# Optimization experiments

Measured on AMD Instinct MI355X. Metric: run time of the kernel, lower is better.

Reference implementation:

```python
import jax, jax.numpy as jnp
import numpy as np

E = 1_000_000
C = 32
OUT = 64


def setup_inputs() -> dict:
    key = jax.random.key(0)
    k_x, k_nb, k_w, k_b = jax.random.split(key, 4)
    x = jax.random.normal(k_x, (E, C), dtype=jnp.float32)
    neighbors = jax.random.randint(k_nb, (E, 4), 0, E, dtype=jnp.int64)
    # Linear(5*C, OUT): weight [OUT, 5C], bias [OUT] (torch layout)
    bound = 1.0 / np.sqrt(5 * C)
    W = jax.random.uniform(k_w, (OUT, 5 * C), minval=-bound, maxval=bound, dtype=jnp.float32)
    b = jax.random.uniform(k_b, (OUT,), minval=-bound, maxval=bound, dtype=jnp.float32)
    return {"x": x, "neighbors": neighbors, "W": W, "b": b}


def reference(x, neighbors, W, b):
    # pad with a zero row so index -1 (clamped to 0 then masked) yields zeros
    padded = jnp.concatenate([x, jnp.zeros((1, x.shape[1]), dtype=x.dtype)], axis=0)
    safe = jnp.clip(neighbors, 0, None)
    nb = padded[safe]                                  # [E, 4, C]
    nb = jnp.where((neighbors < 0)[..., None], 0.0, nb)
    a0, a1, b0, b1 = nb[:, 0], nb[:, 1], nb[:, 2], nb[:, 3]
    desc_a = jnp.concatenate([a0 + a1, jnp.abs(a0 - a1)], axis=1)   # [E, 2C]
    desc_b = jnp.concatenate([b0 + b1, jnp.abs(b0 - b1)], axis=1)   # [E, 2C]
    combined = jnp.concatenate([x, desc_a + desc_b, jnp.abs(desc_a - desc_b)], axis=1)  # [E, 5C]
    return combined @ W.T + b
```

## Files before the change

### kernel.cpp

```cpp
#include <hip/hip_runtime.h>


typedef __bf16 bf16_t;
typedef __bf16 bf16x8 __attribute__((ext_vector_type(8)));
typedef float  f32x4  __attribute__((ext_vector_type(4)));

#define EC      1000000
#define CCH     32
#define OUTD    64
#define KD      160
#define MT      64
#define NTILES  (EC / MT)
#define NFRAG   1280
#define TSTR    68
#define GRID    1024

__global__ __launch_bounds__(256)
void meshconv_kernel(const float* __restrict__ x,
                     const int*   __restrict__ nbr,
                     const float* __restrict__ W,
                     const float* __restrict__ bias,
                     float*       __restrict__ out)
{
    __shared__ bf16_t w_lds[NFRAG * 8];
    __shared__ __attribute__((aligned(16))) float t_lds[4 * 16 * TSTR];

    const int tid  = threadIdx.x;
    const int wave = tid >> 6;
    const int lane = tid & 63;
    const int col  = lane & 15;
    const int quad = lane >> 4;

    for (int i = tid; i < NFRAG; i += 256) {
        const int fc  = i & 15;
        const int fq  = (i >> 4) & 3;
        const int ftn = (i >> 6) & 3;
        const int fks = i >> 8;
        const float* src = W + (ftn * 16 + fc) * KD + fks * 32 + fq * 8;
        f32x4 w0 = *(const f32x4*)src;
        f32x4 w1 = *(const f32x4*)(src + 4);
        bf16x8 wf;
        wf[0]=(bf16_t)w0[0]; wf[1]=(bf16_t)w0[1]; wf[2]=(bf16_t)w0[2]; wf[3]=(bf16_t)w0[3];
        wf[4]=(bf16_t)w1[0]; wf[5]=(bf16_t)w1[1]; wf[6]=(bf16_t)w1[2]; wf[7]=(bf16_t)w1[3];
        *(bf16x8*)&w_lds[i * 8] = wf;
    }

    float bv[4];
#pragma unroll
    for (int tn = 0; tn < 4; ++tn) bv[tn] = bias[tn * 16 + col];

    float* tw = &t_lds[wave * 16 * TSTR];

    __syncthreads();

    auto load_tile = [&](int t, int4& nb, f32x4* buf) {
        const int e = t * MT + wave * 16 + col;
        nb = ((const int4*)nbr)[e];
        const int i0 = nb.x < 0 ? 0 : nb.x;
        const int i1 = nb.y < 0 ? 0 : nb.y;
        const int i2 = nb.z < 0 ? 0 : nb.z;
        const int i3 = nb.w < 0 ? 0 : nb.w;
        const int co = quad * 8;
        const f32x4* p;
        p = (const f32x4*)(x + (size_t)e  * CCH + co); buf[0] = p[0]; buf[1] = p[1];
        p = (const f32x4*)(x + (size_t)i0 * CCH + co); buf[2] = p[0]; buf[3] = p[1];
        p = (const f32x4*)(x + (size_t)i1 * CCH + co); buf[4] = p[0]; buf[5] = p[1];
        p = (const f32x4*)(x + (size_t)i2 * CCH + co); buf[6] = p[0]; buf[7] = p[1];
        p = (const f32x4*)(x + (size_t)i3 * CCH + co); buf[8] = p[0]; buf[9] = p[1];
    };

    int tile = blockIdx.x;
    int4  nbc;
    f32x4 cb[10];
    if (tile < NTILES) load_tile(tile, nbc, cb);

    for (; tile < NTILES; tile += GRID) {
        const int nxt = tile + GRID;
        int4  nbn;
        f32x4 pb[10];
        if (nxt < NTILES) load_tile(nxt, nbn, pb);

        const float m0 = nbc.x < 0 ? 0.f : 1.f;
        const float m1 = nbc.y < 0 ? 0.f : 1.f;
        const float m2 = nbc.z < 0 ? 0.f : 1.f;
        const float m3 = nbc.w < 0 ? 0.f : 1.f;

        bf16x8 af[5];
#pragma unroll
        for (int h = 0; h < 2; ++h) {
#pragma unroll
            for (int j = 0; j < 4; ++j) {
                const int jj = h * 4 + j;
                const float va0 = cb[2 + h][j] * m0;
                const float va1 = cb[4 + h][j] * m1;
                const float vb0 = cb[6 + h][j] * m2;
                const float vb1 = cb[8 + h][j] * m3;
                const float sa = va0 + va1;
                const float da = fabsf(va0 - va1);
                const float sb = vb0 + vb1;
                const float db = fabsf(vb0 - vb1);
                af[0][jj] = (bf16_t)cb[h][j];
                af[1][jj] = (bf16_t)(sa + sb);
                af[2][jj] = (bf16_t)(da + db);
                af[3][jj] = (bf16_t)fabsf(sa - sb);
                af[4][jj] = (bf16_t)fabsf(da - db);
            }
        }

        f32x4 acc[4] = {{0.f,0.f,0.f,0.f},{0.f,0.f,0.f,0.f},
                        {0.f,0.f,0.f,0.f},{0.f,0.f,0.f,0.f}};
#pragma unroll
        for (int ks = 0; ks < 5; ++ks) {
#pragma unroll
            for (int tn = 0; tn < 4; ++tn) {
                const bf16x8 bfr = *(const bf16x8*)&w_lds[(((ks*4+tn)*4+quad)*16 + col) * 8];
                acc[tn] = __builtin_amdgcn_mfma_f32_16x16x32_bf16(af[ks], bfr, acc[tn], 0, 0, 0);
            }
        }

#pragma unroll
        for (int tn = 0; tn < 4; ++tn)
#pragma unroll
            for (int r = 0; r < 4; ++r)
                tw[(quad * 4 + r) * TSTR + tn * 16 + col] = acc[tn][r] + bv[tn];

#pragma unroll
        for (int r = 0; r < 4; ++r) {
            const f32x4 v = *(const f32x4*)&tw[(quad * 4 + r) * TSTR + col * 4];
            float* op = out + (size_t)(tile * MT + wave * 16 + quad * 4 + r) * OUTD + col * 4;
            __builtin_nontemporal_store(v, (f32x4*)op);
        }

        nbc = nbn;
#pragma unroll
        for (int k = 0; k < 10; ++k) cb[k] = pb[k];
    }
}

extern "C" void kernel_launch(void* const* d_in, const int* in_sizes, int n_in,
                              void* d_out, int out_size, void* d_ws, size_t ws_size,
                              hipStream_t stream) {
    const float* x    = (const float*)d_in[0];
    const int*   nbr  = (const int*)d_in[1];
    const float* W    = (const float*)d_in[2];
    const float* bias = (const float*)d_in[3];
    float* out = (float*)d_out;
    meshconv_kernel<<<dim3(GRID), dim3(256), 0, stream>>>(x, nbr, W, bias, out);
}
```

Measured before the change: 410.9 us.

## Pre-convert x to fp16 in workspace and gather half-width rows

Adds a pre-pass kernel that converts x to fp16 in the workspace. The main kernel then gathers 64-byte rows instead of 128-byte rows, which halves the bytes moved by the random neighbor gathers. The MFMA operands are swapped so each lane holds output rows directly, removing the LDS transpose before the stores, and bias is preloaded into the accumulators. In exchange it adds a full extra read/write pass over x and a second launch, and it loses precision from storing x in fp16. The old fp32 kernel is kept as a fallback when the workspace is too small.

Result: slower. 667.7 us (+62.5%).

```diff
diff --git a/kernel.cpp b/kernel.cpp
--- a/kernel.cpp
+++ b/kernel.cpp
@@ -1,19 +1,160 @@
 #include <hip/hip_runtime.h>
 
 
-typedef __bf16 bf16_t;
-typedef __bf16 bf16x8 __attribute__((ext_vector_type(8)));
-typedef float  f32x4  __attribute__((ext_vector_type(4)));
-
-#define EC      1000000
-#define CCH     32
-#define OUTD    64
-#define KD      160
-#define MT      64
-#define NTILES  (EC / MT)
-#define NFRAG   1280
-#define TSTR    68
-#define GRID    1024
+typedef __bf16    bf16_t;
+typedef __bf16    bf16x8 __attribute__((ext_vector_type(8)));
+typedef _Float16  f16_t;
+typedef _Float16  f16x8  __attribute__((ext_vector_type(8)));
+typedef float     f32x4  __attribute__((ext_vector_type(4)));
+
+#define EC        1000000
+#define CCH       32
+#define OUTD      64
+#define KD        160
+#define MT        64
+#define NTILES    (EC / MT)
+#define NFRAG     1280
+#define GRID_F16  1536
+#define CVT_GRID  2048
+#define TSTR      68
+#define GRID_F32  1024
+
+__global__ __launch_bounds__(256)
+void cvt_x_f16(const float* __restrict__ x, f16_t* __restrict__ xh)
+{
+    const size_t n8     = (size_t)EC * CCH / 8;
+    const size_t stride = (size_t)CVT_GRID * 256;
+    size_t i = (size_t)blockIdx.x * 256 + threadIdx.x;
+    for (; i < n8; i += stride) {
+        const f32x4* p = (const f32x4*)x + 2 * i;
+        f32x4 a = __builtin_nontemporal_load(p);
+        f32x4 b = __builtin_nontemporal_load(p + 1);
+        f16x8 h;
+        h[0]=(f16_t)a[0]; h[1]=(f16_t)a[1]; h[2]=(f16_t)a[2]; h[3]=(f16_t)a[3];
+        h[4]=(f16_t)b[0]; h[5]=(f16_t)b[1]; h[6]=(f16_t)b[2]; h[7]=(f16_t)b[3];
+        *((f16x8*)xh + i) = h;
+    }
+}
+
+__global__ __launch_bounds__(256, 6)
+void meshconv_f16(const f16_t* __restrict__ xh,
+                  const int*   __restrict__ nbr,
+                  const float* __restrict__ W,
+                  const float* __restrict__ bias,
+                  float*       __restrict__ out)
+{
+    __shared__ bf16_t w_lds[NFRAG * 8];
+    __shared__ __attribute__((aligned(16))) float b_lds[OUTD];
+
+    const int tid  = threadIdx.x;
+    const int wave = tid >> 6;
+    const int lane = tid & 63;
+    const int col  = lane & 15;
+    const int quad = lane >> 4;
+
+    for (int i = tid; i < NFRAG; i += 256) {
+        const int fc  = i & 15;
+        const int fq  = (i >> 4) & 3;
+        const int ftn = (i >> 6) & 3;
+        const int fks = i >> 8;
+        const float* src = W + (ftn * 16 + fc) * KD + fks * 32 + fq * 8;
+        f32x4 w0 = *(const f32x4*)src;
+        f32x4 w1 = *(const f32x4*)(src + 4);
+        bf16x8 wf;
+        wf[0]=(bf16_t)w0[0]; wf[1]=(bf16_t)w0[1]; wf[2]=(bf16_t)w0[2]; wf[3]=(bf16_t)w0[3];
+        wf[4]=(bf16_t)w1[0]; wf[5]=(bf16_t)w1[1]; wf[6]=(bf16_t)w1[2]; wf[7]=(bf16_t)w1[3];
+        *(bf16x8*)&w_lds[i * 8] = wf;
+    }
+    if (tid < 16) *(f32x4*)&b_lds[tid * 4] = ((const f32x4*)bias)[tid];
+
+    __syncthreads();
+
+    auto ld_nbr = [&](int t) -> int4 {
+        return ((const int4*)nbr)[t * MT + wave * 16 + col];
+    };
+    auto gather = [&](int t, const int4& nb, f16x8* buf) {
+        const int e  = t * MT + wave * 16 + col;
+        const int i0 = nb.x < 0 ? 0 : nb.x;
+        const int i1 = nb.y < 0 ? 0 : nb.y;
+        const int i2 = nb.z < 0 ? 0 : nb.z;
+        const int i3 = nb.w < 0 ? 0 : nb.w;
+        const int co = quad * 8;
+        buf[0] = *(const f16x8*)(xh + (size_t)e  * CCH + co);
+        buf[1] = *(const f16x8*)(xh + (size_t)i0 * CCH + co);
+        buf[2] = *(const f16x8*)(xh + (size_t)i1 * CCH + co);
+        buf[3] = *(const f16x8*)(xh + (size_t)i2 * CCH + co);
+        buf[4] = *(const f16x8*)(xh + (size_t)i3 * CCH + co);
+    };
+
+    int tile = blockIdx.x;
+    int4  nb_cur, nb_nxt;
+    f16x8 cb[5];
+    if (tile < NTILES) {
+        nb_cur = ld_nbr(tile);
+        gather(tile, nb_cur, cb);
+        const int t1 = (tile + GRID_F16 < NTILES) ? tile + GRID_F16 : tile;
+        nb_nxt = ld_nbr(t1);
+    }
+
+    for (; tile < NTILES; tile += GRID_F16) {
+        const int nxt = tile + GRID_F16;
+        f16x8 pb[5];
+        int4  nb2 = nb_nxt;
+        if (nxt < NTILES) {
+            gather(nxt, nb_nxt, pb);
+            const int t2 = (nxt + GRID_F16 < NTILES) ? nxt + GRID_F16 : nxt;
+            nb2 = ld_nbr(t2);
+        }
+
+        const float m0 = nb_cur.x < 0 ? 0.f : 1.f;
+        const float m1 = nb_cur.y < 0 ? 0.f : 1.f;
+        const float m2 = nb_cur.z < 0 ? 0.f : 1.f;
+        const float m3 = nb_cur.w < 0 ? 0.f : 1.f;
+
+        bf16x8 af[5];
+#pragma unroll
+        for (int jj = 0; jj < 8; ++jj) {
+            const float va0 = (float)cb[1][jj] * m0;
+            const float va1 = (float)cb[2][jj] * m1;
+            const float vb0 = (float)cb[3][jj] * m2;
+            const float vb1 = (float)cb[4][jj] * m3;
+            const float sa = va0 + va1;
+            const float da = fabsf(va0 - va1);
+            const float sb = vb0 + vb1;
+            const float db = fabsf(vb0 - vb1);
+            af[0][jj] = (bf16_t)(float)cb[0][jj];
+            af[1][jj] = (bf16_t)(sa + sb);
+            af[2][jj] = (bf16_t)(da + db);
+            af[3][jj] = (bf16_t)fabsf(sa - sb);
+            af[4][jj] = (bf16_t)fabsf(da - db);
+        }
+
+        f32x4 acc[4];
+#pragma unroll
+        for (int tn = 0; tn < 4; ++tn)
+            acc[tn] = *(const f32x4*)&b_lds[tn * 16 + quad * 4];
+#pragma unroll
+        for (int ks = 0; ks < 5; ++ks) {
+#pragma unroll
+            for (int tn = 0; tn < 4; ++tn) {
+                const bf16x8 wfr = *(const bf16x8*)&w_lds[(((ks*4+tn)*4+quad)*16 + col) * 8];
+                acc[tn] = __builtin_amdgcn_mfma_f32_16x16x32_bf16(wfr, af[ks], acc[tn], 0, 0, 0);
+            }
+        }
+
+        {
+            float* ob = out + (size_t)(tile * MT + wave * 16 + col) * OUTD + quad * 4;
+#pragma unroll
+            for (int tn = 0; tn < 4; ++tn)
+                __builtin_nontemporal_store(acc[tn], (f32x4*)(ob + tn * 16));
+        }
+
+        nb_cur = nb_nxt;
+        nb_nxt = nb2;
+#pragma unroll
+        for (int k = 0; k < 5; ++k) cb[k] = pb[k];
+    }
+}
 
 __global__ __launch_bounds__(256)
 void meshconv_kernel(const float* __restrict__ x,
@@ -74,11 +215,11 @@
     f32x4 cb[10];
     if (tile < NTILES) load_tile(tile, nbc, cb);
 
-    for (; tile < NTILES; tile += GRID) {
-        const int nxt = tile + GRID;
+    for (; tile < NTILES; tile += GRID_F32) {
+        const int nxt = tile + GRID_F32;
         int4  nbn;
-        f32x4 pb[10];
-        if (nxt < NTILES) load_tile(nxt, nbn, pb);
+        f32x4 pbuf[10];
+        if (nxt < NTILES) load_tile(nxt, nbn, pbuf);
 
         const float m0 = nbc.x < 0 ? 0.f : 1.f;
         const float m1 = nbc.y < 0 ? 0.f : 1.f;
@@ -133,7 +274,7 @@
 
         nbc = nbn;
 #pragma unroll
-        for (int k = 0; k < 10; ++k) cb[k] = pb[k];
+        for (int k = 0; k < 10; ++k) cb[k] = pbuf[k];
     }
 }
 
@@ -145,5 +286,13 @@
     const float* W    = (const float*)d_in[2];
     const float* bias = (const float*)d_in[3];
     float* out = (float*)d_out;
-    meshconv_kernel<<<dim3(GRID), dim3(256), 0, stream>>>(x, nbr, W, bias, out);
-}
+
+    const size_t need = (size_t)EC * CCH * sizeof(f16_t);
+    if (d_ws != nullptr && ws_size >= need) {
+        f16_t* xh = (f16_t*)d_ws;
+        cvt_x_f16<<<dim3(CVT_GRID), dim3(256), 0, stream>>>(x, xh);
+        meshconv_f16<<<dim3(GRID_F16), dim3(256), 0, stream>>>(xh, nbr, W, bias, out);
+    } else {
+        meshconv_kernel<<<dim3(GRID_F32), dim3(256), 0, stream>>>(x, nbr, W, bias, out);
+    }
+}
```

## Cut registers and LDS to raise occupancy, restructure gather prefetch

Applied to the files above, without the earlier changes.

The single-tile register double buffer (cb/pb) is replaced. The current tile's gathered rows are converted to bf16 fragments first, then the next tile's gather is issued into the same registers before the MFMAs run, and neighbor indices are prefetched two tiles ahead. The LDS transpose staging shrinks from 16 rows to 4 rows per wave by writing quad by quad, and launch bounds request 5 blocks per CU with a larger grid. The goal is higher occupancy to hide random-gather latency. The cost is a shorter prefetch distance and a serialized store loop that relies on compiler barriers in place of explicit wave synchronization.

Result: slower. 554.9 us (+35.0%).

```diff
diff --git a/kernel.cpp b/kernel.cpp
--- a/kernel.cpp
+++ b/kernel.cpp
@@ -13,9 +13,9 @@
 #define NTILES  (EC / MT)
 #define NFRAG   1280
 #define TSTR    68
-#define GRID    1024
+#define GRID    1280
 
-__global__ __launch_bounds__(256)
+__global__ __launch_bounds__(256, 5)
 void meshconv_kernel(const float* __restrict__ x,
                      const int*   __restrict__ nbr,
                      const float* __restrict__ W,
@@ -23,7 +23,7 @@
                      float*       __restrict__ out)
 {
     __shared__ bf16_t w_lds[NFRAG * 8];
-    __shared__ __attribute__((aligned(16))) float t_lds[4 * 16 * TSTR];
+    __shared__ __attribute__((aligned(16))) float t_lds[4 * 4 * TSTR];
 
     const int tid  = threadIdx.x;
     const int wave = tid >> 6;
@@ -49,13 +49,15 @@
 #pragma unroll
     for (int tn = 0; tn < 4; ++tn) bv[tn] = bias[tn * 16 + col];
 
-    float* tw = &t_lds[wave * 16 * TSTR];
+    float* tw = &t_lds[wave * 4 * TSTR];
 
     __syncthreads();
 
-    auto load_tile = [&](int t, int4& nb, f32x4* buf) {
-        const int e = t * MT + wave * 16 + col;
-        nb = ((const int4*)nbr)[e];
+    auto ld_nbr = [&](int t) -> int4 {
+        return ((const int4*)nbr)[t * MT + wave * 16 + col];
+    };
+    auto gather = [&](int t, const int4& nb, f32x4* buf) {
+        const int e  = t * MT + wave * 16 + col;
         const int i0 = nb.x < 0 ? 0 : nb.x;
         const int i1 = nb.y < 0 ? 0 : nb.y;
         const int i2 = nb.z < 0 ? 0 : nb.z;
@@ -70,20 +72,20 @@
     };
 
     int tile = blockIdx.x;
-    int4  nbc;
+    int4  nb_cur, nb_nxt;
     f32x4 cb[10];
-    if (tile < NTILES) load_tile(tile, nbc, cb);
+    if (tile < NTILES) {
+        nb_cur = ld_nbr(tile);
+        gather(tile, nb_cur, cb);
+        const int t1 = (tile + GRID < NTILES) ? tile + GRID : tile;
+        nb_nxt = ld_nbr(t1);
+    }
 
     for (; tile < NTILES; tile += GRID) {
-        const int nxt = tile + GRID;
-        int4  nbn;
-        f32x4 pb[10];
-        if (nxt < NTILES) load_tile(nxt, nbn, pb);
-
-        const float m0 = nbc.x < 0 ? 0.f : 1.f;
-        const float m1 = nbc.y < 0 ? 0.f : 1.f;
-        const float m2 = nbc.z < 0 ? 0.f : 1.f;
-        const float m3 = nbc.w < 0 ? 0.f : 1.f;
+        const float m0 = nb_cur.x < 0 ? 0.f : 1.f;
+        const float m1 = nb_cur.y < 0 ? 0.f : 1.f;
+        const float m2 = nb_cur.z < 0 ? 0.f : 1.f;
+        const float m3 = nb_cur.w < 0 ? 0.f : 1.f;
 
         bf16x8 af[5];
 #pragma unroll
@@ -107,6 +109,14 @@
             }
         }
 
+        const int nxt = tile + GRID;
+        int4 nb2 = nb_nxt;
+        if (nxt < NTILES) {
+            gather(nxt, nb_nxt, cb);
+            const int t2 = (nxt + GRID < NTILES) ? nxt + GRID : nxt;
+            nb2 = ld_nbr(t2);
+        }
+
         f32x4 acc[4] = {{0.f,0.f,0.f,0.f},{0.f,0.f,0.f,0.f},
                         {0.f,0.f,0.f,0.f},{0.f,0.f,0.f,0.f}};
 #pragma unroll
@@ -119,21 +129,23 @@
         }
 
 #pragma unroll
-        for (int tn = 0; tn < 4; ++tn)
+        for (int p = 0; p < 4; ++p) {
+            if (quad == p) {
 #pragma unroll
-            for (int r = 0; r < 4; ++r)
-                tw[(quad * 4 + r) * TSTR + tn * 16 + col] = acc[tn][r] + bv[tn];
-
+                for (int tn = 0; tn < 4; ++tn)
 #pragma unroll
-        for (int r = 0; r < 4; ++r) {
-            const f32x4 v = *(const f32x4*)&tw[(quad * 4 + r) * TSTR + col * 4];
-            float* op = out + (size_t)(tile * MT + wave * 16 + quad * 4 + r) * OUTD + col * 4;
+                    for (int r = 0; r < 4; ++r)
+                        tw[r * TSTR + tn * 16 + col] = acc[tn][r] + bv[tn];
+            }
+            asm volatile("" ::: "memory");
+            const f32x4 v = *(const f32x4*)&tw[quad * TSTR + col * 4];
+            asm volatile("" ::: "memory");
+            float* op = out + (size_t)(tile * MT + wave * 16 + p * 4 + quad) * OUTD + col * 4;
             __builtin_nontemporal_store(v, (f32x4*)op);
         }
 
-        nbc = nbn;
-#pragma unroll
-        for (int k = 0; k < 10; ++k) cb[k] = pb[k];
+        nb_cur = nb_nxt;
+        nb_nxt = nb2;
     }
 }
 
```
